# Kernel tuning notes

Measured on AMD Instinct MI355X. Metric: run time of the kernel, lower is better.

Reference implementation:

```python
import jax, jax.numpy as jnp
import numpy as np

BN_EPS = 1e-5

def conv1x1(x, w, b):
    # x: [B,C,H,W], w: [O,C], b: [O] -> [B,O,H,W]
    return jnp.einsum('bchw,oc->bohw', x, w) + b[None, :, None, None]

def setup_inputs() -> dict:
    key = jax.random.key(0)
    ks = jax.random.split(key, 12)
    B, C, H, W = 16, 512, 64, 32
    Ch = C // 2  # hidden_channel
    s = 0.02
    return {
        'x':       jax.random.normal(ks[0], (B, C, H, W), jnp.float32),
        'theta_w': jax.random.normal(ks[1], (Ch, C), jnp.float32) * s,
        'theta_b': jax.random.normal(ks[2], (Ch,), jnp.float32) * s,
        'phi_w':   jax.random.normal(ks[3], (Ch, C), jnp.float32) * s,
        'phi_b':   jax.random.normal(ks[4], (Ch,), jnp.float32) * s,
        'g_w':     jax.random.normal(ks[5], (Ch, C), jnp.float32) * s,
        'g_b':     jax.random.normal(ks[6], (Ch,), jnp.float32) * s,
        'W_w':     jax.random.normal(ks[7], (C, Ch), jnp.float32) * s,
        'W_b':     jax.random.normal(ks[8], (C,), jnp.float32) * s,
        'bn_gamma': 1.0 + jax.random.normal(ks[9], (C,), jnp.float32) * 0.1,
        'bn_beta':  jax.random.normal(ks[10], (C,), jnp.float32) * 0.1,
    }

def reference(x, theta_w, theta_b, phi_w, phi_b, g_w, g_b, W_w, W_b, bn_gamma, bn_beta):
    B, C, H, Wd = x.shape
    N = H * Wd
    Ch = theta_w.shape[0]
    # 1x1 conv projections, flattened over spatial dims
    th = conv1x1(x, theta_w, theta_b).reshape(B, Ch, N)  # theta: [B,Ch,N]
    ph = conv1x1(x, phi_w, phi_b).reshape(B, Ch, N)      # phi:   [B,Ch,N]
    gv = conv1x1(x, g_w, g_b).reshape(B, Ch, N)          # g:     [B,Ch,N]
    # dense affinity (no softmax), normalized by N, as in the original
    f = jnp.einsum('bcn,bcm->bnm', th, ph) / N           # [B,N,N]
    y = jnp.einsum('bnm,bcm->bcn', f, gv).reshape(B, Ch, H, Wd)
    # W: 1x1 conv + BatchNorm2d (training-mode batch statistics, biased var)
    w = conv1x1(y, W_w, W_b)                             # [B,C,H,W]
    mean = w.mean(axis=(0, 2, 3), keepdims=True)
    var = w.var(axis=(0, 2, 3), keepdims=True)
    wn = (w - mean) * jax.lax.rsqrt(var + BN_EPS)
    wn = wn * bn_gamma[None, :, None, None] + bn_beta[None, :, None, None]
    return wn + x
```

## Files before the change

### kernel.cpp

```cpp
#include <hip/hip_runtime.h>

typedef __bf16 bf16x8 __attribute__((ext_vector_type(8)));
typedef float floatx4 __attribute__((ext_vector_type(4)));

#define DEVI __device__ __forceinline__

DEVI unsigned short f2bf(float f) {
  union { float f; unsigned u; } v; v.f = f;
  unsigned r = v.u + 0x7FFFu + ((v.u >> 16) & 1u);
  return (unsigned short)(r >> 16);
}

DEVI void gload_lds16(const void* g, void* l) {
  __builtin_amdgcn_global_load_lds((const __attribute__((address_space(1))) void*)g,
                                   (__attribute__((address_space(3))) void*)l,
                                   16, 0, 0);
}

__global__ __launch_bounds__(256) void k_transpose(
    const float* __restrict__ x, unsigned short* __restrict__ xt,
    const float* __restrict__ phi_w, const float* __restrict__ g_w,
    const float* __restrict__ theta_w, const float* __restrict__ W_w,
    const float* __restrict__ phi_b, const float* __restrict__ g_b,
    unsigned short* __restrict__ wpg, unsigned short* __restrict__ thw,
    unsigned short* __restrict__ ww, float* __restrict__ pgbias) {
  const int t = threadIdx.x;
  if (blockIdx.z == 16) {
    const int T0 = 512 * 512, T1 = T0 + 256 * 512, T2 = T1 + 512 * 256, T3 = T2 + 512;
    int base = (blockIdx.y * 32 + blockIdx.x) * 256 + t;
    for (int i = base; i < T3; i += 65536) {
      if (i < T0) {
        int o = i >> 9, c = i & 511;
        float v = (o < 256) ? phi_w[o * 512 + c] : g_w[(o - 256) * 512 + c];
        wpg[i] = f2bf(v);
      } else if (i < T1) {
        int j = i - T0; thw[j] = f2bf(theta_w[j]);
      } else if (i < T2) {
        int j = i - T1; ww[j] = f2bf(W_w[j]);
      } else {
        int o = i - T2; pgbias[o] = (o < 256) ? phi_b[o] : g_b[o - 256];
      }
    }
    return;
  }
  __shared__ float tile[64][65];
  const int b = blockIdx.z, c0 = blockIdx.y * 64, n0 = blockIdx.x * 64;
  const float* xb = x + (size_t)b * 512 * 2048;
#pragma unroll
  for (int i = 0; i < 16; ++i) {
    int lin = i * 256 + t;
    int lc = lin >> 6, ln = lin & 63;
    tile[lc][ln] = xb[(size_t)(c0 + lc) * 2048 + (n0 + ln)];
  }
  __syncthreads();
  unsigned short* xtb = xt + (size_t)b * 2048 * 512;
#pragma unroll
  for (int i = 0; i < 16; ++i) {
    int lin = i * 256 + t;
    int ln = lin >> 6, lc = lin & 63;
    xtb[(size_t)(n0 + ln) * 512 + (c0 + lc)] = f2bf(tile[lc][ln]);
  }
}

template <int BM, int BN, int EPI>
__global__ __launch_bounds__(256) void k_gemm(
    const unsigned short* __restrict__ A, const unsigned short* __restrict__ B,
    unsigned short* __restrict__ C, int N, int K,
    size_t sA, size_t sB, size_t sC,
    const float* __restrict__ bias, float scale) {
  constexpr int WM = BM / 2, WN = BN / 2;
  constexpr int FM = WM / 16, FN = WN / 16;
  __shared__ __align__(16) __bf16 At[BM * 64];
  __shared__ __align__(16) __bf16 Bt[BN * 64];
  const int t = threadIdx.x;
  const int z = blockIdx.z;
  const int row0 = blockIdx.y * BM, col0 = blockIdx.x * BN;
  const unsigned short* Az = A + (size_t)z * sA;
  const unsigned short* Bz = B + (size_t)z * sB;
  unsigned short* Cz = C + (size_t)z * sC;

  const int w = t >> 6, lane = t & 63;
  const int l16 = lane & 15, lq = lane >> 4;
  const int wrow0 = (w >> 1) * WM, wcol0 = (w & 1) * WN;
  const int xorb = (l16 & 7) << 4;
  const int aoff0 = (wrow0 + l16) * 128;
  const int boff0 = (wcol0 + l16) * 128;

  floatx4 acc[FM][FN];
#pragma unroll
  for (int m = 0; m < FM; ++m)
#pragma unroll
    for (int n = 0; n < FN; ++n) acc[m][n] = (floatx4){0.f, 0.f, 0.f, 0.f};

  const int kt_end = K >> 6;
  for (int kt = 0; kt < kt_end; ++kt) {
    __syncthreads();
#pragma unroll
    for (int i = 0; i < BM * 8 / 256; ++i) {
      int ch = i * 256 + t;
      int r = ch >> 3;
      int sc = ((((ch & 7) << 4) ^ ((r & 7) << 4)) >> 1);
      gload_lds16(Az + (size_t)(row0 + r) * K + (kt << 6) + sc, &At[ch * 8]);
    }
#pragma unroll
    for (int i = 0; i < BN * 8 / 256; ++i) {
      int ch = i * 256 + t;
      int r = ch >> 3;
      int sc = ((((ch & 7) << 4) ^ ((r & 7) << 4)) >> 1);
      gload_lds16(Bz + (size_t)(col0 + r) * K + (kt << 6) + sc, &Bt[ch * 8]);
    }
    __syncthreads();

#pragma unroll
    for (int kk = 0; kk < 2; ++kk) {
      const int ck = ((kk << 6) + (lq << 4)) ^ xorb;
      bf16x8 af[FM], bq[FN];
#pragma unroll
      for (int m = 0; m < FM; ++m)
        af[m] = *(const bf16x8*)((const char*)At + aoff0 + m * 2048 + ck);
#pragma unroll
      for (int n = 0; n < FN; ++n)
        bq[n] = *(const bf16x8*)((const char*)Bt + boff0 + n * 2048 + ck);
#pragma unroll
      for (int m = 0; m < FM; ++m)
#pragma unroll
        for (int n = 0; n < FN; ++n)
          acc[m][n] = __builtin_amdgcn_mfma_f32_16x16x32_bf16(af[m], bq[n], acc[m][n], 0, 0, 0);
    }
  }

#pragma unroll
  for (int m = 0; m < FM; ++m)
#pragma unroll
    for (int n = 0; n < FN; ++n) {
      int gc = col0 + wcol0 + n * 16 + l16;
      float bc = (EPI == 2) ? bias[gc] : 0.f;
#pragma unroll
      for (int r = 0; r < 4; ++r) {
        int gr = row0 + wrow0 + m * 16 + lq * 4 + r;
        float v = acc[m][n][r] * scale;
        if (EPI == 1) v += bias[gr];
        if (EPI == 2) v += bc;
        Cz[(size_t)gr * N + gc] = f2bf(v);
      }
    }
}

__global__ __launch_bounds__(256) void k_gemm_part(const unsigned short* __restrict__ phg,
                                                   float* __restrict__ pbuf) {
  __shared__ __align__(16) __bf16 At[128 * 64];
  __shared__ __align__(16) __bf16 Bt[128 * 64];
  const int t = threadIdx.x;
  const int tid = blockIdx.x, b = blockIdx.z;
  const int split = tid >> 2, tr = (tid >> 1) & 1, tc = tid & 1;
  const int row0 = tr * 128, col0 = tc * 128;
  const size_t sPG = (size_t)512 * 2048;
  const unsigned short* Az = phg + (size_t)b * sPG + (size_t)row0 * 2048;
  const unsigned short* Bz = phg + (size_t)b * sPG + (size_t)(256 + col0) * 2048;
  const int w = t >> 6, lane = t & 63;
  const int l16 = lane & 15, lq = lane >> 4;
  const int wrow0 = (w >> 1) * 64, wcol0 = (w & 1) * 64;
  const int xorb = (l16 & 7) << 4;
  const int aoff0 = (wrow0 + l16) * 128;
  const int boff0 = (wcol0 + l16) * 128;

  floatx4 acc[4][4];
#pragma unroll
  for (int m = 0; m < 4; ++m)
#pragma unroll
    for (int n = 0; n < 4; ++n) acc[m][n] = (floatx4){0.f, 0.f, 0.f, 0.f};

  for (int kt8 = 0; kt8 < 8; ++kt8) {
    const int kt = split * 8 + kt8;
    __syncthreads();
#pragma unroll
    for (int i = 0; i < 4; ++i) {
      int ch = i * 256 + t;
      int r = ch >> 3;
      int sc = ((((ch & 7) << 4) ^ ((r & 7) << 4)) >> 1);
      gload_lds16(Az + (size_t)r * 2048 + (kt << 6) + sc, &At[ch * 8]);
    }
#pragma unroll
    for (int i = 0; i < 4; ++i) {
      int ch = i * 256 + t;
      int r = ch >> 3;
      int sc = ((((ch & 7) << 4) ^ ((r & 7) << 4)) >> 1);
      gload_lds16(Bz + (size_t)r * 2048 + (kt << 6) + sc, &Bt[ch * 8]);
    }
    __syncthreads();
#pragma unroll
    for (int kk = 0; kk < 2; ++kk) {
      const int ck = ((kk << 6) + (lq << 4)) ^ xorb;
      bf16x8 af[4], bq[4];
#pragma unroll
      for (int m = 0; m < 4; ++m)
        af[m] = *(const bf16x8*)((const char*)At + aoff0 + m * 2048 + ck);
#pragma unroll
      for (int n = 0; n < 4; ++n)
        bq[n] = *(const bf16x8*)((const char*)Bt + boff0 + n * 2048 + ck);
#pragma unroll
      for (int m = 0; m < 4; ++m)
#pragma unroll
        for (int n = 0; n < 4; ++n)
          acc[m][n] = __builtin_amdgcn_mfma_f32_16x16x32_bf16(af[m], bq[n], acc[m][n], 0, 0, 0);
    }
  }
  float* outp = pbuf + ((size_t)split * 16 + b) * 65536;
#pragma unroll
  for (int m = 0; m < 4; ++m)
#pragma unroll
    for (int n = 0; n < 4; ++n)
#pragma unroll
      for (int r = 0; r < 4; ++r) {
        int gr = row0 + wrow0 + m * 16 + lq * 4 + r;
        int gc = col0 + wcol0 + n * 16 + l16;
        outp[(size_t)gr * 256 + gc] = acc[m][n][r];
      }
}

__global__ __launch_bounds__(256) void k_gemm_f32b(const unsigned short* __restrict__ ww,
                                                   const float* __restrict__ pbuf,
                                                   unsigned short* __restrict__ mmat) {
  __shared__ __align__(16) __bf16 At[64 * 32];
  __shared__ __align__(16) __bf16 Bt[64 * 32];
  const int t = threadIdx.x;
  const int b = blockIdx.z;
  const int col0 = blockIdx.x * 64;
  const int row0 = blockIdx.y * 64;
  const size_t SSTR = (size_t)16 * 65536;
  const float* Bz = pbuf + (size_t)b * 65536;
  const int w = t >> 6, lane = t & 63;
  const int l16 = lane & 15, lq = lane >> 4;
  const int wrow0 = (w >> 1) * 32, wcol0 = (w & 1) * 32;

  floatx4 acc[2][2];
#pragma unroll
  for (int m = 0; m < 2; ++m)
#pragma unroll
    for (int n = 0; n < 2; ++n) acc[m][n] = (floatx4){0.f, 0.f, 0.f, 0.f};

  for (int kt = 0; kt < 8; ++kt) {
    __syncthreads();
    {
      int r = t >> 2, kq = t & 3;
      gload_lds16(ww + (size_t)(row0 + r) * 256 + (kt << 5) + (kq << 3), &At[t * 8]);
    }
    {
      int r = t >> 2, kq = t & 3;
      const float* src = Bz + (size_t)(col0 + r) * 256 + (kt << 5) + (kq << 3);
      float4 a = *(const float4*)src;
      float4 c = *(const float4*)(src + 4);
#pragma unroll
      for (int s = 1; s < 4; ++s) {
        float4 a2 = *(const float4*)(src + s * SSTR);
        float4 c2 = *(const float4*)(src + s * SSTR + 4);
        a.x += a2.x; a.y += a2.y; a.z += a2.z; a.w += a2.w;
        c.x += c2.x; c.y += c2.y; c.z += c2.z; c.w += c2.w;
      }
      union { unsigned short s[8]; bf16x8 v; } pk;
      pk.s[0] = f2bf(a.x); pk.s[1] = f2bf(a.y); pk.s[2] = f2bf(a.z); pk.s[3] = f2bf(a.w);
      pk.s[4] = f2bf(c.x); pk.s[5] = f2bf(c.y); pk.s[6] = f2bf(c.z); pk.s[7] = f2bf(c.w);
      *(bf16x8*)&Bt[t * 8] = pk.v;
    }
    __syncthreads();
    bf16x8 af[2], bq[2];
#pragma unroll
    for (int m = 0; m < 2; ++m)
      af[m] = *(const bf16x8*)&At[(wrow0 + m * 16 + l16) * 32 + lq * 8];
#pragma unroll
    for (int n = 0; n < 2; ++n)
      bq[n] = *(const bf16x8*)&Bt[(wcol0 + n * 16 + l16) * 32 + lq * 8];
#pragma unroll
    for (int m = 0; m < 2; ++m)
#pragma unroll
      for (int n = 0; n < 2; ++n)
        acc[m][n] = __builtin_amdgcn_mfma_f32_16x16x32_bf16(af[m], bq[n], acc[m][n], 0, 0, 0);
  }
  unsigned short* Cz = mmat + (size_t)b * 512 * 256;
  const float scale = 1.f / 2048.f;
#pragma unroll
  for (int m = 0; m < 2; ++m)
#pragma unroll
    for (int n = 0; n < 2; ++n)
#pragma unroll
      for (int r = 0; r < 4; ++r) {
        int gr = row0 + wrow0 + m * 16 + lq * 4 + r;
        int gc = col0 + wcol0 + n * 16 + l16;
        Cz[(size_t)gr * 256 + gc] = f2bf(acc[m][n][r] * scale);
      }
}

__global__ __launch_bounds__(256) void k_bnstats(const unsigned short* __restrict__ w,
                                                 const float* __restrict__ gamma,
                                                 const float* __restrict__ beta,
                                                 float* __restrict__ scale,
                                                 float* __restrict__ shift) {
  const int c = blockIdx.x, t = threadIdx.x;
  float s = 0.f, ss = 0.f;
  for (int b = 0; b < 16; ++b) {
    const unsigned short* p = w + ((size_t)b * 512 + c) * 2048 + t * 8;
    uint4 v = *(const uint4*)p;
    unsigned u[4] = {v.x, v.y, v.z, v.w};
#pragma unroll
    for (int j = 0; j < 4; ++j) {
      union { unsigned q; float f; } a, bb;
      a.q = u[j] << 16;
      bb.q = u[j] & 0xFFFF0000u;
      s += a.f + bb.f;
      ss += a.f * a.f + bb.f * bb.f;
    }
  }
#pragma unroll
  for (int off = 32; off; off >>= 1) {
    s += __shfl_down(s, off);
    ss += __shfl_down(ss, off);
  }
  __shared__ float ls[4], lss[4];
  if ((t & 63) == 0) { ls[t >> 6] = s; lss[t >> 6] = ss; }
  __syncthreads();
  if (t == 0) {
    float S = ls[0] + ls[1] + ls[2] + ls[3];
    float SS = lss[0] + lss[1] + lss[2] + lss[3];
    const float inv = 1.f / 32768.f;
    float mean = S * inv;
    float var = SS * inv - mean * mean;
    float rs = rsqrtf(var + 1e-5f);
    float sc = gamma[c] * rs;
    scale[c] = sc;
    shift[c] = beta[c] - mean * sc;
  }
}

__global__ __launch_bounds__(256) void k_final(const unsigned short* __restrict__ w,
                                               const float* __restrict__ x,
                                               const float* __restrict__ scale,
                                               const float* __restrict__ shift,
                                               float* __restrict__ out) {
  const size_t total4 = (size_t)16 * 512 * 2048 / 4;
  size_t stride = (size_t)gridDim.x * 256;
  for (size_t i = (size_t)blockIdx.x * 256 + threadIdx.x; i < total4; i += stride) {
    size_t e = i * 4;
    int c = (int)((e >> 11) & 511);
    float sc = scale[c], sh = shift[c];
    uint2 wv = *(const uint2*)(w + e);
    float4 xv = *(const float4*)(x + e);
    float4 o;
    union { unsigned q; float f; } a;
    a.q = wv.x << 16;          o.x = a.f * sc + sh + xv.x;
    a.q = wv.x & 0xFFFF0000u;  o.y = a.f * sc + sh + xv.y;
    a.q = wv.y << 16;          o.z = a.f * sc + sh + xv.z;
    a.q = wv.y & 0xFFFF0000u;  o.w = a.f * sc + sh + xv.w;
    *(float4*)(out + e) = o;
  }
}

extern "C" void kernel_launch(void* const* d_in, const int* in_sizes, int n_in,
                              void* d_out, int out_size, void* d_ws, size_t ws_size,
                              hipStream_t stream) {
  const float* x       = (const float*)d_in[0];
  const float* theta_w = (const float*)d_in[1];
  const float* theta_b = (const float*)d_in[2];
  const float* phi_w   = (const float*)d_in[3];
  const float* phi_b   = (const float*)d_in[4];
  const float* g_w     = (const float*)d_in[5];
  const float* g_b     = (const float*)d_in[6];
  const float* W_w     = (const float*)d_in[7];
  const float* W_b     = (const float*)d_in[8];
  const float* gamma   = (const float*)d_in[9];
  const float* beta    = (const float*)d_in[10];
  float* out = (float*)d_out;

  char* ws = (char*)d_ws;
  size_t off = 0;
  auto alloc = [&](size_t bytes) {
    char* p = ws + off;
    off = (off + bytes + 255) & ~(size_t)255;
    return p;
  };
  unsigned short* xt    = (unsigned short*)alloc((size_t)16 * 2048 * 512 * 2);
  unsigned short* phg   = (unsigned short*)alloc((size_t)16 * 512 * 2048 * 2);
  unsigned short* tht   = (unsigned short*)alloc((size_t)16 * 2048 * 256 * 2);
  float*          pbuf  = (float*)alloc((size_t)4 * 16 * 256 * 256 * 4);
  unsigned short* mmat  = (unsigned short*)alloc((size_t)16 * 512 * 256 * 2);
  unsigned short* wbuf  = (unsigned short*)alloc((size_t)16 * 512 * 2048 * 2);
  unsigned short* wpg   = (unsigned short*)alloc((size_t)512 * 512 * 2);
  unsigned short* thw   = (unsigned short*)alloc((size_t)256 * 512 * 2);
  unsigned short* ww    = (unsigned short*)alloc((size_t)512 * 256 * 2);
  float* pgbias         = (float*)alloc(512 * 4);
  float* scalev         = (float*)alloc(512 * 4);
  float* shiftv         = (float*)alloc(512 * 4);
  (void)ws_size; (void)in_sizes; (void)n_in; (void)out_size;

  const size_t sXT = (size_t)2048 * 512;
  const size_t sPG = (size_t)512 * 2048;
  const size_t sTH = (size_t)2048 * 256;
  const size_t sMM = (size_t)512 * 256;
  const size_t sW  = (size_t)512 * 2048;

  k_transpose<<<dim3(32, 8, 17), 256, 0, stream>>>(x, xt, phi_w, g_w, theta_w, W_w,
                                                   phi_b, g_b, wpg, thw, ww, pgbias);

  k_gemm<128, 128, 1><<<dim3(16, 4, 16), 256, 0, stream>>>(
      wpg, xt, phg, 2048, 512, 0, sXT, sPG, pgbias, 1.f);
  k_gemm<128, 128, 2><<<dim3(2, 16, 16), 256, 0, stream>>>(
      xt, thw, tht, 256, 512, sXT, 0, sTH, theta_b, 1.f);
  k_gemm_part<<<dim3(16, 1, 16), 256, 0, stream>>>(phg, pbuf);
  k_gemm_f32b<<<dim3(4, 8, 16), 256, 0, stream>>>(ww, pbuf, mmat);
  k_gemm<128, 128, 1><<<dim3(16, 4, 16), 256, 0, stream>>>(
      mmat, tht, wbuf, 2048, 256, sMM, sTH, sW, W_b, 1.f);

  k_bnstats<<<512, 256, 0, stream>>>(wbuf, gamma, beta, scalev, shiftv);
  k_final<<<4096, 256, 0, stream>>>(wbuf, x, scalev, shiftv, out);
}
```

Measured before the change: 253.1 us.

## Replace GEMMs with 256x256 pipelined 8-wave kernel and merge projection launches

Replaces the 128x128 single-buffered GEMM kernels with a shared 256x256-tile, 512-thread body. It uses a 4-slot LDS ring with async global-to-LDS loads staged one k-step ahead, explicit vmcnt waits, barriers and MFMA priority raising. The phi/g and theta projections are merged into one launch. The phi·g^T split-K is widened from 4 to 16 splits, so the f32 partial buffer and its reduction loop grow. The aim is better MFMA utilization and latency hiding, at the cost of 128KB of LDS per block, higher register pressure, and fewer blocks for some GEMMs.

```diff
diff --git a/kernel.cpp b/kernel.cpp
--- a/kernel.cpp
+++ b/kernel.cpp
@@ -62,160 +62,149 @@
   }
 }
 
-template <int BM, int BN, int EPI>
-__global__ __launch_bounds__(256) void k_gemm(
-    const unsigned short* __restrict__ A, const unsigned short* __restrict__ B,
-    unsigned short* __restrict__ C, int N, int K,
-    size_t sA, size_t sB, size_t sC,
-    const float* __restrict__ bias, float scale) {
-  constexpr int WM = BM / 2, WN = BN / 2;
-  constexpr int FM = WM / 16, FN = WN / 16;
-  __shared__ __align__(16) __bf16 At[BM * 64];
-  __shared__ __align__(16) __bf16 Bt[BN * 64];
+
+#define VMC4 asm volatile("s_waitcnt vmcnt(4)" ::: "memory");
+#define VMC0 asm volatile("s_waitcnt vmcnt(0)" ::: "memory");
+#define VMNO
+
+#define PHASE(RING, MH, SR, SK, C0, VM)                                          \
+  {                                                                              \
+    bf16x8 af[4], bq[4];                                                         \
+    _Pragma("unroll") for (int m = 0; m < 4; ++m) {                              \
+      int ra = wr * 128 + ((MH) * 4 + m) * 16 + l16;                             \
+      af[m] = *(const bf16x8*)(lds + ((RING) << 15) + ra * 64 +                  \
+                               ((lq << 4) ^ (((ra >> 1) & 3) << 4)));            \
+    }                                                                            \
+    _Pragma("unroll") for (int n = 0; n < 4; ++n) {                              \
+      int rb = 256 + wc * 64 + n * 16 + l16;                                     \
+      bq[n] = *(const bf16x8*)(lds + ((RING) << 15) + rb * 64 +                  \
+                               ((lq << 4) ^ (((rb >> 1) & 3) << 4)));            \
+    }                                                                            \
+    if ((SR) >= 0) {                                                             \
+      stage_chunk((SR), (SK), kt + 1, (C0));                                     \
+      stage_chunk((SR), (SK), kt + 1, (C0) + 1);                                 \
+    }                                                                            \
+    VM                                                                           \
+    __builtin_amdgcn_s_barrier();                                                \
+    asm volatile("s_waitcnt lgkmcnt(0)" ::: "memory");                           \
+    __builtin_amdgcn_sched_barrier(0);                                           \
+    __builtin_amdgcn_s_setprio(1);                                               \
+    _Pragma("unroll") for (int m = 0; m < 4; ++m)                                \
+      _Pragma("unroll") for (int n = 0; n < 4; ++n)                              \
+        acc[(MH) * 4 + m][n] = __builtin_amdgcn_mfma_f32_16x16x32_bf16(          \
+            af[m], bq[n], acc[(MH) * 4 + m][n], 0, 0, 0);                        \
+    __builtin_amdgcn_s_setprio(0);                                               \
+    __builtin_amdgcn_s_barrier();                                                \
+  }
+
+template <int EPI, bool F32OUT>
+DEVI void gemm256_body(const unsigned short* __restrict__ Ap,
+                       const unsigned short* __restrict__ Bp,
+                       void* __restrict__ Cp, int ldc, int K, int k0, int nt,
+                       int row0, int col0, const float* __restrict__ bias,
+                       float scale, char* lds) {
   const int t = threadIdx.x;
-  const int z = blockIdx.z;
-  const int row0 = blockIdx.y * BM, col0 = blockIdx.x * BN;
-  const unsigned short* Az = A + (size_t)z * sA;
-  const unsigned short* Bz = B + (size_t)z * sB;
-  unsigned short* Cz = C + (size_t)z * sC;
-
-  const int w = t >> 6, lane = t & 63;
-  const int l16 = lane & 15, lq = lane >> 4;
-  const int wrow0 = (w >> 1) * WM, wcol0 = (w & 1) * WN;
-  const int xorb = (l16 & 7) << 4;
-  const int aoff0 = (wrow0 + l16) * 128;
-  const int boff0 = (wcol0 + l16) * 128;
-
-  floatx4 acc[FM][FN];
-#pragma unroll
-  for (int m = 0; m < FM; ++m)
-#pragma unroll
-    for (int n = 0; n < FN; ++n) acc[m][n] = (floatx4){0.f, 0.f, 0.f, 0.f};
-
-  const int kt_end = K >> 6;
-  for (int kt = 0; kt < kt_end; ++kt) {
-    __syncthreads();
-#pragma unroll
-    for (int i = 0; i < BM * 8 / 256; ++i) {
-      int ch = i * 256 + t;
-      int r = ch >> 3;
-      int sc = ((((ch & 7) << 4) ^ ((r & 7) << 4)) >> 1);
-      gload_lds16(Az + (size_t)(row0 + r) * K + (kt << 6) + sc, &At[ch * 8]);
-    }
-#pragma unroll
-    for (int i = 0; i < BN * 8 / 256; ++i) {
-      int ch = i * 256 + t;
-      int r = ch >> 3;
-      int sc = ((((ch & 7) << 4) ^ ((r & 7) << 4)) >> 1);
-      gload_lds16(Bz + (size_t)(col0 + r) * K + (kt << 6) + sc, &Bt[ch * 8]);
-    }
-    __syncthreads();
-
-#pragma unroll
-    for (int kk = 0; kk < 2; ++kk) {
-      const int ck = ((kk << 6) + (lq << 4)) ^ xorb;
-      bf16x8 af[FM], bq[FN];
-#pragma unroll
-      for (int m = 0; m < FM; ++m)
-        af[m] = *(const bf16x8*)((const char*)At + aoff0 + m * 2048 + ck);
-#pragma unroll
-      for (int n = 0; n < FN; ++n)
-        bq[n] = *(const bf16x8*)((const char*)Bt + boff0 + n * 2048 + ck);
-#pragma unroll
-      for (int m = 0; m < FM; ++m)
-#pragma unroll
-        for (int n = 0; n < FN; ++n)
-          acc[m][n] = __builtin_amdgcn_mfma_f32_16x16x32_bf16(af[m], bq[n], acc[m][n], 0, 0, 0);
-    }
-  }
-
-#pragma unroll
-  for (int m = 0; m < FM; ++m)
-#pragma unroll
-    for (int n = 0; n < FN; ++n) {
-      int gc = col0 + wcol0 + n * 16 + l16;
+  const int w = t >> 6, l = t & 63;
+  const int l16 = l & 15, lq = l >> 4;
+  const int wr = w >> 2, wc = w & 3;
+
+  floatx4 acc[8][4];
+#pragma unroll
+  for (int m = 0; m < 8; ++m)
+#pragma unroll
+    for (int n = 0; n < 4; ++n) acc[m][n] = (floatx4){0.f, 0.f, 0.f, 0.f};
+
+  auto stage_chunk = [&](int ring, int kk, int skt, int c) {
+    int row = (c * 8 + w) * 16 + (l >> 2);
+    int slot = l & 3;
+    int ksub = slot ^ ((row >> 1) & 3);
+    int kcol = k0 + (skt << 6) + (kk << 5) + (ksub << 3);
+    const unsigned short* src = (row < 256)
+        ? Ap + (size_t)(row0 + row) * K + kcol
+        : Bp + (size_t)(col0 + row - 256) * K + kcol;
+    gload_lds16(src, lds + (ring << 15) + (((c * 8 + w) << 6) + l) * 16);
+  };
+
+#pragma unroll
+  for (int c = 0; c < 4; ++c) stage_chunk(0, 0, 0, c);
+#pragma unroll
+  for (int c = 0; c < 4; ++c) stage_chunk(1, 1, 0, c);
+  VMC4
+  __builtin_amdgcn_s_barrier();
+
+  for (int kt = 0; kt < nt; ++kt) {
+    const int r0 = (2 * kt) & 3, r1 = (2 * kt + 1) & 3;
+    const int s0 = (2 * kt + 2) & 3, s1 = (2 * kt + 3) & 3;
+    if (kt + 1 < nt) {
+      PHASE(r0, 0, s0, 0, 0, VMNO)
+      PHASE(r0, 1, s0, 0, 2, VMC4)
+      PHASE(r1, 0, s1, 1, 0, VMNO)
+      PHASE(r1, 1, s1, 1, 2, VMC4)
+    } else {
+      PHASE(r0, 0, -1, 0, 0, VMNO)
+      PHASE(r0, 1, -1, 0, 0, VMC0)
+      PHASE(r1, 0, -1, 0, 0, VMNO)
+      PHASE(r1, 1, -1, 0, 0, VMNO)
+    }
+  }
+
+#pragma unroll
+  for (int m = 0; m < 8; ++m)
+#pragma unroll
+    for (int n = 0; n < 4; ++n) {
+      int gc = col0 + wc * 64 + n * 16 + l16;
       float bc = (EPI == 2) ? bias[gc] : 0.f;
 #pragma unroll
       for (int r = 0; r < 4; ++r) {
-        int gr = row0 + wrow0 + m * 16 + lq * 4 + r;
+        int gr = row0 + wr * 128 + m * 16 + lq * 4 + r;
         float v = acc[m][n][r] * scale;
         if (EPI == 1) v += bias[gr];
         if (EPI == 2) v += bc;
-        Cz[(size_t)gr * N + gc] = f2bf(v);
+        if (F32OUT)
+          ((float*)Cp)[(size_t)gr * ldc + gc] = v;
+        else
+          ((unsigned short*)Cp)[(size_t)gr * ldc + gc] = f2bf(v);
       }
     }
 }
 
-__global__ __launch_bounds__(256) void k_gemm_part(const unsigned short* __restrict__ phg,
-                                                   float* __restrict__ pbuf) {
-  __shared__ __align__(16) __bf16 At[128 * 64];
-  __shared__ __align__(16) __bf16 Bt[128 * 64];
-  const int t = threadIdx.x;
-  const int tid = blockIdx.x, b = blockIdx.z;
-  const int split = tid >> 2, tr = (tid >> 1) & 1, tc = tid & 1;
-  const int row0 = tr * 128, col0 = tc * 128;
+__global__ __launch_bounds__(512, 2) void k_proj8(
+    const unsigned short* __restrict__ wpg, const unsigned short* __restrict__ xt,
+    const unsigned short* __restrict__ thw,
+    unsigned short* __restrict__ phg, unsigned short* __restrict__ tht,
+    const float* __restrict__ pgbias, const float* __restrict__ theta_b) {
+  __shared__ __align__(16) char lds[131072];
+  const int x = blockIdx.x, z = blockIdx.z;
+  const size_t sXT = (size_t)2048 * 512, sPG = (size_t)512 * 2048, sTH = (size_t)2048 * 256;
+  if (x < 16) {
+    gemm256_body<1, false>(wpg, xt + z * sXT, phg + z * sPG, 2048, 512, 0, 8,
+                           (x >> 3) * 256, (x & 7) * 256, pgbias, 1.f, lds);
+  } else {
+    const int u = x - 16;
+    gemm256_body<2, false>(xt + z * sXT, thw, tht + z * sTH, 256, 512, 0, 8,
+                           u * 256, 0, theta_b, 1.f, lds);
+  }
+}
+
+__global__ __launch_bounds__(512, 2) void k_part8(const unsigned short* __restrict__ phg,
+                                                  float* __restrict__ pbuf) {
+  __shared__ __align__(16) char lds[131072];
+  const int split = blockIdx.x, b = blockIdx.z;
   const size_t sPG = (size_t)512 * 2048;
-  const unsigned short* Az = phg + (size_t)b * sPG + (size_t)row0 * 2048;
-  const unsigned short* Bz = phg + (size_t)b * sPG + (size_t)(256 + col0) * 2048;
-  const int w = t >> 6, lane = t & 63;
-  const int l16 = lane & 15, lq = lane >> 4;
-  const int wrow0 = (w >> 1) * 64, wcol0 = (w & 1) * 64;
-  const int xorb = (l16 & 7) << 4;
-  const int aoff0 = (wrow0 + l16) * 128;
-  const int boff0 = (wcol0 + l16) * 128;
-
-  floatx4 acc[4][4];
-#pragma unroll
-  for (int m = 0; m < 4; ++m)
-#pragma unroll
-    for (int n = 0; n < 4; ++n) acc[m][n] = (floatx4){0.f, 0.f, 0.f, 0.f};
-
-  for (int kt8 = 0; kt8 < 8; ++kt8) {
-    const int kt = split * 8 + kt8;
-    __syncthreads();
-#pragma unroll
-    for (int i = 0; i < 4; ++i) {
-      int ch = i * 256 + t;
-      int r = ch >> 3;
-      int sc = ((((ch & 7) << 4) ^ ((r & 7) << 4)) >> 1);
-      gload_lds16(Az + (size_t)r * 2048 + (kt << 6) + sc, &At[ch * 8]);
-    }
-#pragma unroll
-    for (int i = 0; i < 4; ++i) {
-      int ch = i * 256 + t;
-      int r = ch >> 3;
-      int sc = ((((ch & 7) << 4) ^ ((r & 7) << 4)) >> 1);
-      gload_lds16(Bz + (size_t)r * 2048 + (kt << 6) + sc, &Bt[ch * 8]);
-    }
-    __syncthreads();
-#pragma unroll
-    for (int kk = 0; kk < 2; ++kk) {
-      const int ck = ((kk << 6) + (lq << 4)) ^ xorb;
-      bf16x8 af[4], bq[4];
-#pragma unroll
-      for (int m = 0; m < 4; ++m)
-        af[m] = *(const bf16x8*)((const char*)At + aoff0 + m * 2048 + ck);
-#pragma unroll
-      for (int n = 0; n < 4; ++n)
-        bq[n] = *(const bf16x8*)((const char*)Bt + boff0 + n * 2048 + ck);
-#pragma unroll
-      for (int m = 0; m < 4; ++m)
-#pragma unroll
-        for (int n = 0; n < 4; ++n)
-          acc[m][n] = __builtin_amdgcn_mfma_f32_16x16x32_bf16(af[m], bq[n], acc[m][n], 0, 0, 0);
-    }
-  }
-  float* outp = pbuf + ((size_t)split * 16 + b) * 65536;
-#pragma unroll
-  for (int m = 0; m < 4; ++m)
-#pragma unroll
-    for (int n = 0; n < 4; ++n)
-#pragma unroll
-      for (int r = 0; r < 4; ++r) {
-        int gr = row0 + wrow0 + m * 16 + lq * 4 + r;
-        int gc = col0 + wcol0 + n * 16 + l16;
-        outp[(size_t)gr * 256 + gc] = acc[m][n][r];
-      }
+  gemm256_body<0, true>(phg + (size_t)b * sPG, phg + (size_t)b * sPG + (size_t)256 * 2048,
+                        pbuf + ((size_t)split * 16 + b) * 65536, 256,
+                        2048, split * 128, 2, 0, 0, nullptr, 1.f, lds);
+}
+
+__global__ __launch_bounds__(512, 2) void k_gemm58(const unsigned short* __restrict__ mmat,
+                                                   const unsigned short* __restrict__ tht,
+                                                   unsigned short* __restrict__ wbuf,
+                                                   const float* __restrict__ W_b) {
+  __shared__ __align__(16) char lds[131072];
+  const int x = blockIdx.x, z = blockIdx.z;
+  const size_t sMM = (size_t)512 * 256, sTH = (size_t)2048 * 256, sW = (size_t)512 * 2048;
+  gemm256_body<1, false>(mmat + z * sMM, tht + z * sTH, wbuf + z * sW, 2048, 256, 0, 4,
+                         (x >> 3) * 256, (x & 7) * 256, W_b, 1.f, lds);
 }
 
 __global__ __launch_bounds__(256) void k_gemm_f32b(const unsigned short* __restrict__ ww,
@@ -251,7 +240,7 @@
       float4 a = *(const float4*)src;
       float4 c = *(const float4*)(src + 4);
 #pragma unroll
-      for (int s = 1; s < 4; ++s) {
+      for (int s = 1; s < 16; ++s) {
         float4 a2 = *(const float4*)(src + s * SSTR);
         float4 c2 = *(const float4*)(src + s * SSTR + 4);
         a.x += a2.x; a.y += a2.y; a.z += a2.z; a.w += a2.w;
@@ -380,7 +369,7 @@
   unsigned short* xt    = (unsigned short*)alloc((size_t)16 * 2048 * 512 * 2);
   unsigned short* phg   = (unsigned short*)alloc((size_t)16 * 512 * 2048 * 2);
   unsigned short* tht   = (unsigned short*)alloc((size_t)16 * 2048 * 256 * 2);
-  float*          pbuf  = (float*)alloc((size_t)4 * 16 * 256 * 256 * 4);
+  float*          pbuf  = (float*)alloc((size_t)16 * 16 * 256 * 256 * 4);
   unsigned short* mmat  = (unsigned short*)alloc((size_t)16 * 512 * 256 * 2);
   unsigned short* wbuf  = (unsigned short*)alloc((size_t)16 * 512 * 2048 * 2);
   unsigned short* wpg   = (unsigned short*)alloc((size_t)512 * 512 * 2);
@@ -391,24 +380,12 @@
   float* shiftv         = (float*)alloc(512 * 4);
   (void)ws_size; (void)in_sizes; (void)n_in; (void)out_size;
 
-  const size_t sXT = (size_t)2048 * 512;
-  const size_t sPG = (size_t)512 * 2048;
-  const size_t sTH = (size_t)2048 * 256;
-  const size_t sMM = (size_t)512 * 256;
-  const size_t sW  = (size_t)512 * 2048;
-
   k_transpose<<<dim3(32, 8, 17), 256, 0, stream>>>(x, xt, phi_w, g_w, theta_w, W_w,
                                                    phi_b, g_b, wpg, thw, ww, pgbias);
-
-  k_gemm<128, 128, 1><<<dim3(16, 4, 16), 256, 0, stream>>>(
-      wpg, xt, phg, 2048, 512, 0, sXT, sPG, pgbias, 1.f);
-  k_gemm<128, 128, 2><<<dim3(2, 16, 16), 256, 0, stream>>>(
-      xt, thw, tht, 256, 512, sXT, 0, sTH, theta_b, 1.f);
-  k_gemm_part<<<dim3(16, 1, 16), 256, 0, stream>>>(phg, pbuf);
+  k_proj8<<<dim3(24, 1, 16), 512, 0, stream>>>(wpg, xt, thw, phg, tht, pgbias, theta_b);
+  k_part8<<<dim3(16, 1, 16), 512, 0, stream>>>(phg, pbuf);
   k_gemm_f32b<<<dim3(4, 8, 16), 256, 0, stream>>>(ww, pbuf, mmat);
-  k_gemm<128, 128, 1><<<dim3(16, 4, 16), 256, 0, stream>>>(
-      mmat, tht, wbuf, 2048, 256, sMM, sTH, sW, W_b, 1.f);
-
+  k_gemm58<<<dim3(16, 1, 16), 512, 0, stream>>>(mmat, tht, wbuf, W_b);
   k_bnstats<<<512, 256, 0, stream>>>(wbuf, gamma, beta, scalev, shiftv);
   k_final<<<4096, 256, 0, stream>>>(wbuf, x, scalev, shiftv, out);
 }
```

New measurement: 282.8 us. +11.7%, slower.
